# Optimization experiments

Measured on AMD Instinct MI355X. Metric: run time of the kernel, lower is better.

Reference implementation:

```python
import jax, jax.numpy as jnp
import numpy as np
import math

EPS = 1e-5

def layernorm(x, g, b):
    mu = jnp.mean(x, axis=-1, keepdims=True)
    var = jnp.var(x, axis=-1, keepdims=True)
    return (x - mu) * jax.lax.rsqrt(var + EPS) * g + b

def setup_inputs() -> dict:
    key = jax.random.key(0)
    ks = jax.random.split(key, 12)
    B, T, E, H = 4, 2048, 128, 8
    D = H * E          # 1024
    F = 4 * D          # 4096
    s = 0.02
    return {
        "X":     jax.random.normal(ks[0], (B, T, E), jnp.float32),
        "ln1_g": jnp.ones((E,), jnp.float32),
        "ln1_b": jnp.zeros((E,), jnp.float32),
        "Wq":    jax.random.normal(ks[1], (H, E, E), jnp.float32) * s,
        "bq":    jax.random.normal(ks[2], (H, E), jnp.float32) * s,
        "Wk":    jax.random.normal(ks[3], (H, E, E), jnp.float32) * s,
        "bk":    jax.random.normal(ks[4], (H, E), jnp.float32) * s,
        "Wv":    jax.random.normal(ks[5], (H, E, E), jnp.float32) * s,
        "bv":    jax.random.normal(ks[6], (H, E), jnp.float32) * s,
        "ln2_g": jnp.ones((D,), jnp.float32),
        "ln2_b": jnp.zeros((D,), jnp.float32),
        "W1":    jax.random.normal(ks[7], (D, F), jnp.float32) * s,
        "b1":    jax.random.normal(ks[8], (F,), jnp.float32) * s,
        "W2":    jax.random.normal(ks[9], (F, E), jnp.float32) * s,
        "b2":    jax.random.normal(ks[10], (E,), jnp.float32) * s,
    }

def reference(X, ln1_g, ln1_b, Wq, bq, Wk, bk, Wv, bv, ln2_g, ln2_b, W1, b1, W2, b2):
    B, T, E = X.shape
    Xn = layernorm(X, ln1_g, ln1_b)                       # [B,T,E]
    # per-head projections, vectorized over heads
    q = jnp.einsum('bte,hef->bhtf', Xn, Wq) + bq[None, :, None, :]
    k = jnp.einsum('bte,hef->bhtf', Xn, Wk) + bk[None, :, None, :]
    v = jnp.einsum('bte,hef->bhtf', Xn, Wv) + bv[None, :, None, :]
    scores = jnp.einsum('bhtf,bhsf->bhts', q, k) / math.sqrt(E)
    # causal mask: positions with s > t set to -inf (triu offset=1)
    t_idx = jnp.arange(T)
    mask = t_idx[None, :] > t_idx[:, None]                # [T,S], True above diag
    scores = jnp.where(mask[None, None], -jnp.inf, scores)
    # NOTE: original code softmaxes over dim = ndim-2, i.e. the QUERY axis
    attn = jax.nn.softmax(scores, axis=-2)
    out = jnp.einsum('bhts,bhsf->bhtf', attn, v)          # [B,H,T,E]
    # concat heads along last dim (head order preserved)
    concat = jnp.transpose(out, (0, 2, 1, 3)).reshape(B, T, -1)  # [B,T,H*E]
    h = layernorm(concat, ln2_g, ln2_b)
    mid = jax.nn.gelu(h @ W1 + b1, approximate=False)
    return mid @ W2 + b2                                   # [B,T,E]
```

## Files before the change

### kernel.cpp

```cpp
#include <hip/hip_runtime.h>
#include <hip/hip_bf16.h>
#include <math.h>

typedef __hip_bfloat16 bf16;
typedef __attribute__((ext_vector_type(8))) short short8;
typedef __attribute__((ext_vector_type(4))) float floatx4;

#define B_ 4
#define T_ 2048
#define E_ 128
#define H_ 8
#define D_ 1024
#define F_ 4096
#define M_ 8192

static __device__ __forceinline__ float b2f(bf16 v){ return __bfloat162float(v); }
static __device__ __forceinline__ bf16  f2b(float v){ return __float2bfloat16(v); }
static __device__ __forceinline__ short f2bs(float v){ bf16 h = __float2bfloat16(v); return *(short*)&h; }

static __device__ __forceinline__ void glds16(const bf16* g, void* l){
  __builtin_amdgcn_global_load_lds((const __attribute__((address_space(1))) void*)g,
                                   (__attribute__((address_space(3))) void*)l, 16, 0, 0);
}

__global__ void detect_dtype_k(const unsigned int* __restrict__ g, int* __restrict__ flag){
  if (threadIdx.x == 0) flag[0] = (g[0] == 0x3F803F80u) ? 1 : 0;
}

__global__ void convert_misc_k(const void* s0, const void* s1, const void* s2, const void* s3,
                               const void* s4, const void* s5, const void* s6, const void* s7,
                               const void* s8,
                               bf16* g1, bf16* b1, bf16* bqkv, bf16* g2, bf16* b2l,
                               bf16* bb1, bf16* bb2, const int* __restrict__ flag){
  int i = blockIdx.x * 256 + threadIdx.x;
  if (i >= 9600) return;
  int fl = flag[0];
  const void* src; bf16* dst; int off;
  if      (i <  128){ src = s0; dst = g1;          off = i;        }
  else if (i <  256){ src = s1; dst = b1;          off = i - 128;  }
  else if (i < 1280){ src = s2; dst = bqkv;        off = i - 256;  }
  else if (i < 2304){ src = s3; dst = bqkv + 1024; off = i - 1280; }
  else if (i < 3328){ src = s4; dst = bqkv + 2048; off = i - 2304; }
  else if (i < 4352){ src = s5; dst = g2;          off = i - 3328; }
  else if (i < 5376){ src = s6; dst = b2l;         off = i - 4352; }
  else if (i < 9472){ src = s7; dst = bb1;         off = i - 5376; }
  else              { src = s8; dst = bb2;         off = i - 9472; }
  dst[off] = fl ? ((const bf16*)src)[off] : f2b(((const float*)src)[off]);
}

__global__ __launch_bounds__(256) void transpose_cvt_k(const void* __restrict__ src, bf16* __restrict__ dst,
                                                       int R, int C, const int* __restrict__ flag){
  __shared__ float tile[32][33];
  int r0 = blockIdx.y * 32, c0 = blockIdx.x * 32;
  int tx = threadIdx.x & 31, ty = threadIdx.x >> 5;
  int fl = flag[0];
  #pragma unroll
  for (int i = 0; i < 32; i += 8){
    size_t idx = (size_t)(r0 + ty + i) * C + c0 + tx;
    tile[ty + i][tx] = fl ? b2f(((const bf16*)src)[idx]) : ((const float*)src)[idx];
  }
  __syncthreads();
  #pragma unroll
  for (int i = 0; i < 32; i += 8){
    dst[(size_t)(c0 + ty + i) * R + r0 + tx] = f2b(tile[tx][ty + i]);
  }
}

__global__ __launch_bounds__(256) void transpose_qkv_k(const void* __restrict__ Wq, const void* __restrict__ Wk,
                                                       const void* __restrict__ Wv, bf16* __restrict__ dst,
                                                       const int* __restrict__ flag){
  __shared__ float tile[32][33];
  int sel = blockIdx.z >> 3, h = blockIdx.z & 7;
  const void* src = (sel == 0) ? Wq : (sel == 1) ? Wk : Wv;
  size_t mo = (size_t)h * E_ * E_;
  bf16* d = dst + (size_t)sel * H_ * E_ * E_ + mo;
  int r0 = blockIdx.y * 32, c0 = blockIdx.x * 32;
  int tx = threadIdx.x & 31, ty = threadIdx.x >> 5;
  int fl = flag[0];
  #pragma unroll
  for (int i = 0; i < 32; i += 8){
    size_t idx = mo + (size_t)(r0 + ty + i) * E_ + c0 + tx;
    tile[ty + i][tx] = fl ? b2f(((const bf16*)src)[idx]) : ((const float*)src)[idx];
  }
  __syncthreads();
  #pragma unroll
  for (int i = 0; i < 32; i += 8){
    d[(size_t)(c0 + ty + i) * E_ + r0 + tx] = f2b(tile[tx][ty + i]);
  }
}

__global__ __launch_bounds__(256) void ln1_k(const void* __restrict__ X, const bf16* __restrict__ g,
                                             const bf16* __restrict__ b, bf16* __restrict__ out,
                                             const int* __restrict__ flag){
  int row = blockIdx.x * 4 + (threadIdx.x >> 6);
  int lane = threadIdx.x & 63;
  float x0, x1;
  if (flag[0]){
    const bf16* xp = (const bf16*)X + (size_t)row * E_;
    x0 = b2f(xp[lane]); x1 = b2f(xp[lane + 64]);
  } else {
    const float* xp = (const float*)X + (size_t)row * E_;
    x0 = xp[lane]; x1 = xp[lane + 64];
  }
  float s  = x0 + x1;
  float s2 = x0 * x0 + x1 * x1;
  #pragma unroll
  for (int o = 32; o > 0; o >>= 1){ s += __shfl_xor(s, o, 64); s2 += __shfl_xor(s2, o, 64); }
  float mu  = s * (1.0f / 128.0f);
  float var = s2 * (1.0f / 128.0f) - mu * mu;
  float rs  = rsqrtf(var + 1e-5f);
  out[(size_t)row * E_ + lane]      = f2b((x0 - mu) * rs * b2f(g[lane])      + b2f(b[lane]));
  out[(size_t)row * E_ + lane + 64] = f2b((x1 - mu) * rs * b2f(g[lane + 64]) + b2f(b[lane + 64]));
}

template<int EPI>
__global__ __launch_bounds__(256, 3) void gemm_mfma_k(
    const bf16* __restrict__ A, const bf16* __restrict__ Bt,
    const bf16* __restrict__ bias, void* __restrict__ out,
    int K, const int* __restrict__ flag)
{
  __shared__ __align__(16) short As[2][4][128][8];
  __shared__ __align__(16) short Bs[2][4][128][8];
  int tid = threadIdx.x;
  int lane = tid & 63, w = tid >> 6;
  int quad = lane >> 4, l16 = lane & 15;
  int wm = w & 1, wn = w >> 1;
  int m0 = blockIdx.y * 128;
  int n0, nit;
  size_t kstart;
  if (EPI == 3){ n0 = 0; int kc = K >> 3; kstart = (size_t)blockIdx.x * kc; nit = kc >> 5; }
  else         { n0 = blockIdx.x * 128; kstart = 0; nit = K >> 5; }

  int seg0 = w * 2, seg1 = w * 2 + 1;
  int kq0 = seg0 & 3, mb0 = (seg0 >> 2) * 64;
  int kq1 = seg1 & 3, mb1 = (seg1 >> 2) * 64;
  const bf16* pa0 = A  + (size_t)(m0 + mb0 + lane) * K + kstart + kq0 * 8;
  const bf16* pa1 = A  + (size_t)(m0 + mb1 + lane) * K + kstart + kq1 * 8;
  const bf16* pb0 = Bt + (size_t)(n0 + mb0 + lane) * K + kstart + kq0 * 8;
  const bf16* pb1 = Bt + (size_t)(n0 + mb1 + lane) * K + kstart + kq1 * 8;
  uint4 ra0 = *(const uint4*)pa0, ra1 = *(const uint4*)pa1;
  uint4 rb0 = *(const uint4*)pb0, rb1 = *(const uint4*)pb1;

  floatx4 acc[4][4];
  #pragma unroll
  for (int i = 0; i < 4; i++)
    #pragma unroll
    for (int j = 0; j < 4; j++) acc[i][j] = (floatx4){0.f, 0.f, 0.f, 0.f};

  for (int it = 0; it < nit; it++){
    int buf = it & 1;
    *(uint4*)&As[buf][kq0][mb0 + lane][0] = ra0;
    *(uint4*)&As[buf][kq1][mb1 + lane][0] = ra1;
    *(uint4*)&Bs[buf][kq0][mb0 + lane][0] = rb0;
    *(uint4*)&Bs[buf][kq1][mb1 + lane][0] = rb1;
    __syncthreads();
    if (it + 1 < nit){
      int ko = (it + 1) << 5;
      ra0 = *(const uint4*)(pa0 + ko); ra1 = *(const uint4*)(pa1 + ko);
      rb0 = *(const uint4*)(pb0 + ko); rb1 = *(const uint4*)(pb1 + ko);
    }
    short8 af[4], bfr[4];
    #pragma unroll
    for (int i = 0; i < 4; i++) af[i]  = *(const short8*)&As[buf][quad][wm * 64 + i * 16 + l16][0];
    #pragma unroll
    for (int j = 0; j < 4; j++) bfr[j] = *(const short8*)&Bs[buf][quad][wn * 64 + j * 16 + l16][0];
    #pragma unroll
    for (int i = 0; i < 4; i++)
      #pragma unroll
      for (int j = 0; j < 4; j++)
        acc[i][j] = __builtin_amdgcn_mfma_f32_16x16x32_bf16(af[i], bfr[j], acc[i][j], 0, 0, 0);
  }

  bf16* po = (EPI == 3) ? (bf16*)out + (size_t)blockIdx.x * M_ * E_ : nullptr;
  #pragma unroll
  for (int i = 0; i < 4; i++){
    #pragma unroll
    for (int j = 0; j < 4; j++){
      int nn = n0 + wn * 64 + j * 16 + l16;
      float bv = (EPI == 3) ? 0.0f : b2f(bias[nn]);
      if (EPI == 0){
        int sel = nn >> 10, h = (nn >> 7) & 7, f = nn & 127;
        size_t SZ = (size_t)B_ * H_ * T_ * E_;
        int mmb = m0 + wm * 64 + i * 16 + quad * 4;
        int b = mmb >> 11, t = mmb & (T_ - 1);
        if (sel < 2){
          #pragma unroll
          for (int r = 0; r < 4; r++)
            ((bf16*)out)[(size_t)sel * SZ + (((size_t)(b * H_ + h) * T_ + t + r) * E_) + f] =
              f2b(acc[i][j][r] + bv);
        } else {
          ushort4 pk;
          #pragma unroll
          for (int r = 0; r < 4; r++) ((short*)&pk)[r] = f2bs(acc[i][j][r] + bv);
          *(ushort4*)((bf16*)out + 2 * SZ + (((size_t)(b * H_ + h) * E_ + f) * T_) + t) = pk;
        }
      } else {
        #pragma unroll
        for (int r = 0; r < 4; r++){
          int mm = m0 + wm * 64 + i * 16 + quad * 4 + r;
          po[(size_t)mm * E_ + nn] = f2b(acc[i][j][r] + bv);
        }
      }
    }
  }
}

__global__ __launch_bounds__(512, 2) void mlp1_8ph_k(
    const bf16* __restrict__ A, const bf16* __restrict__ Bt,
    const bf16* __restrict__ bias, bf16* __restrict__ out)
{
  __shared__ __align__(16) short As[3][4][256][8];
  __shared__ __align__(16) short Bs[3][4][256][8];
  constexpr int K  = D_;
  constexpr int NK = K / 32;

  int tid = threadIdx.x;
  int lane = tid & 63, w = tid >> 6;
  int quad = lane >> 4, l16 = lane & 15;
  int wm = w & 1, wn = w >> 1;
  int m0 = blockIdx.y * 256, n0 = blockIdx.x * 256;

  int u0 = w * 2, u1 = u0 + 1;
  int q0 = u0 & 3, r0 = u0 >> 2;
  int q1 = u1 & 3, r1 = u1 >> 2;
  const bf16* gA0 = A  + (size_t)(m0 + r0 * 64 + lane) * K + q0 * 8;
  const bf16* gA1 = A  + (size_t)(m0 + r1 * 64 + lane) * K + q1 * 8;
  const bf16* gB0 = Bt + (size_t)(n0 + r0 * 64 + lane) * K + q0 * 8;
  const bf16* gB1 = Bt + (size_t)(n0 + r1 * 64 + lane) * K + q1 * 8;

  glds16(gA0,      &As[0][q0][r0 * 64][0]);
  glds16(gA1,      &As[0][q1][r1 * 64][0]);
  glds16(gB0,      &Bs[0][q0][r0 * 64][0]);
  glds16(gB1,      &Bs[0][q1][r1 * 64][0]);
  glds16(gA0 + 32, &As[1][q0][r0 * 64][0]);
  glds16(gA1 + 32, &As[1][q1][r1 * 64][0]);
  glds16(gB0 + 32, &Bs[1][q0][r0 * 64][0]);
  glds16(gB1 + 32, &Bs[1][q1][r1 * 64][0]);
  asm volatile("s_waitcnt vmcnt(4)" ::: "memory");
  __builtin_amdgcn_s_barrier();

  floatx4 acc[2][4][4];
  #pragma unroll
  for (int h = 0; h < 2; h++)
    #pragma unroll
    for (int i = 0; i < 4; i++)
      #pragma unroll
      for (int j = 0; j < 4; j++) acc[h][i][j] = (floatx4){0.f, 0.f, 0.f, 0.f};

  int b0 = 0;
  #pragma unroll 1
  for (int k = 0; k < NK; ++k){
    int b2 = b0 + 2; if (b2 >= 3) b2 -= 3;
    short8 af[4], bf8[4];
    #pragma unroll
    for (int i = 0; i < 4; i++) af[i]  = *(const short8*)&As[b0][quad][wm * 128 + i * 16 + l16][0];
    #pragma unroll
    for (int j = 0; j < 4; j++) bf8[j] = *(const short8*)&Bs[b0][quad][wn * 64  + j * 16 + l16][0];
    if (k + 2 < NK){
      int ko = (k + 2) * 32;
      glds16(gA0 + ko, &As[b2][q0][r0 * 64][0]);
      glds16(gA1 + ko, &As[b2][q1][r1 * 64][0]);
    }
    __builtin_amdgcn_s_barrier();
    __builtin_amdgcn_s_setprio(1);
    #pragma unroll
    for (int i = 0; i < 4; i++)
      #pragma unroll
      for (int j = 0; j < 4; j++)
        acc[0][i][j] = __builtin_amdgcn_mfma_f32_16x16x32_bf16(af[i], bf8[j], acc[0][i][j], 0, 0, 0);
    __builtin_amdgcn_s_setprio(0);
    short8 ah[4];
    #pragma unroll
    for (int i = 0; i < 4; i++) ah[i] = *(const short8*)&As[b0][quad][wm * 128 + 64 + i * 16 + l16][0];
    if (k + 2 < NK){
      int ko = (k + 2) * 32;
      glds16(gB0 + ko, &Bs[b2][q0][r0 * 64][0]);
      glds16(gB1 + ko, &Bs[b2][q1][r1 * 64][0]);
      asm volatile("s_waitcnt vmcnt(4)" ::: "memory");
    } else if (k + 1 < NK){
      asm volatile("s_waitcnt vmcnt(0)" ::: "memory");
    }
    asm volatile("s_waitcnt lgkmcnt(0)" ::: "memory");
    __builtin_amdgcn_sched_barrier(0);
    __builtin_amdgcn_s_barrier();
    __builtin_amdgcn_s_setprio(1);
    #pragma unroll
    for (int i = 0; i < 4; i++)
      #pragma unroll
      for (int j = 0; j < 4; j++)
        acc[1][i][j] = __builtin_amdgcn_mfma_f32_16x16x32_bf16(ah[i], bf8[j], acc[1][i][j], 0, 0, 0);
    __builtin_amdgcn_s_setprio(0);
    b0++; if (b0 == 3) b0 = 0;
  }

  #pragma unroll
  for (int h = 0; h < 2; h++){
    #pragma unroll
    for (int i = 0; i < 4; i++){
      #pragma unroll
      for (int j = 0; j < 4; j++){
        int nn = n0 + wn * 64 + j * 16 + l16;
        float bv = b2f(bias[nn]);
        #pragma unroll
        for (int r = 0; r < 4; r++){
          int mm = m0 + wm * 128 + h * 64 + i * 16 + quad * 4 + r;
          float v = acc[h][i][j][r] + bv;
          float e = __expf(1.5957691216057308f * v * (1.0f + 0.044715f * v * v));
          out[(size_t)mm * F_ + nn] = f2b(v - v / (1.0f + e));
        }
      }
    }
  }
}

__global__ __launch_bounds__(256) void mlp2_fin_k(const bf16* __restrict__ P, const bf16* __restrict__ bias,
                                                  void* __restrict__ out, const int* __restrict__ flag){
  int i = blockIdx.x * 256 + threadIdx.x;
  const size_t S = (size_t)M_ * E_;
  float v = b2f(bias[i & (E_ - 1)]);
  #pragma unroll
  for (int k = 0; k < 8; k++) v += b2f(P[i + k * S]);
  if (flag[0]) ((bf16*)out)[i] = f2b(v);
  else         ((float*)out)[i] = v;
}

__global__ __launch_bounds__(256, 2) void colstats_k(const bf16* __restrict__ Q, const bf16* __restrict__ K,
                                                     float* __restrict__ IL){
  __shared__ __align__(16) short Qs[2][4][4][128][8];
  __shared__ float lcol[64];
  const float scale = 0.0883883476483184f;
  int tid = threadIdx.x;
  int lane = tid & 63, w = tid >> 6;
  int quad = lane >> 4, l16 = lane & 15;
  int x = blockIdx.x;
  int c = x & 255, phase = x >> 8;
  int q = c & 7, bh = c >> 3;
  int sblk = (phase == 0) ? q : (phase == 1) ? 31 - q : (phase == 2) ? 8 + q : 23 - q;
  int s0 = sblk * 64;

  short8 bk[4][4];
  #pragma unroll
  for (int j = 0; j < 4; j++)
    #pragma unroll
    for (int kb = 0; kb < 4; kb++)
      bk[j][kb] = *(const short8*)(K + ((size_t)bh * T_ + s0 + j * 16 + l16) * E_ + kb * 32 + quad * 8);

  if (tid < 64) lcol[tid] = 0.0f;

  int t0s = (s0 / 128) * 128;
  int nit = (T_ - t0s) >> 7;

  #pragma unroll
  for (int t2 = 0; t2 < 8; t2++){
    int seg = w * 8 + t2;
    int kb = seg >> 3, kq = (seg >> 1) & 3, hf = seg & 1;
    const bf16* ga = Q + ((size_t)bh * T_ + t0s + hf * 64 + lane) * E_ + kb * 32 + kq * 8;
    __builtin_amdgcn_global_load_lds((const __attribute__((address_space(1))) void*)ga,
                                     (__attribute__((address_space(3))) void*)&Qs[0][kb][kq][hf * 64][0], 16, 0, 0);
  }
  __syncthreads();

  float part[4] = {0.f, 0.f, 0.f, 0.f};
  for (int it = 0; it < nit; it++){
    int buf = it & 1;
    if (it + 1 < nit){
      int nb = buf ^ 1;
      int t1 = t0s + ((it + 1) << 7);
      #pragma unroll
      for (int t2 = 0; t2 < 8; t2++){
        int seg = w * 8 + t2;
        int kb = seg >> 3, kq = (seg >> 1) & 3, hf = seg & 1;
        const bf16* ga = Q + ((size_t)bh * T_ + t1 + hf * 64 + lane) * E_ + kb * 32 + kq * 8;
        __builtin_amdgcn_global_load_lds((const __attribute__((address_space(1))) void*)ga,
                                         (__attribute__((address_space(3))) void*)&Qs[nb][kb][kq][hf * 64][0], 16, 0, 0);
      }
    }
    floatx4 acc[2][4];
    #pragma unroll
    for (int i = 0; i < 2; i++)
      #pragma unroll
      for (int j = 0; j < 4; j++) acc[i][j] = (floatx4){0.f, 0.f, 0.f, 0.f};
    #pragma unroll
    for (int kb = 0; kb < 4; kb++){
      short8 af[2];
      #pragma unroll
      for (int i = 0; i < 2; i++) af[i] = *(const short8*)&Qs[buf][kb][quad][w * 32 + i * 16 + l16][0];
      #pragma unroll
      for (int i = 0; i < 2; i++)
        #pragma unroll
        for (int j = 0; j < 4; j++)
          acc[i][j] = __builtin_amdgcn_mfma_f32_16x16x32_bf16(af[i], bk[j][kb], acc[i][j], 0, 0, 0);
    }
    int t0 = t0s + (it << 7);
    bool dtile = (it == 0);
    #pragma unroll
    for (int i = 0; i < 2; i++)
      #pragma unroll
      for (int j = 0; j < 4; j++)
        #pragma unroll
        for (int r = 0; r < 4; r++){
          float e = __expf(acc[i][j][r] * scale);
          if (dtile){
            int t = t0 + w * 32 + i * 16 + quad * 4 + r;
            int s = s0 + j * 16 + l16;
            if (t < s) e = 0.0f;
          }
          part[j] += e;
        }
    __syncthreads();
  }
  #pragma unroll
  for (int j = 0; j < 4; j++){
    part[j] += __shfl_xor(part[j], 16, 64);
    part[j] += __shfl_xor(part[j], 32, 64);
  }
  if (quad == 0){
    #pragma unroll
    for (int j = 0; j < 4; j++) atomicAdd(&lcol[j * 16 + l16], part[j]);
  }
  __syncthreads();
  if (tid < 64) IL[(size_t)bh * T_ + s0 + tid] = 1.0f / lcol[tid];
}

__global__ __launch_bounds__(256, 2) void attnout_k(const bf16* __restrict__ Q, const bf16* __restrict__ K,
                                                    const bf16* __restrict__ VT, const float* __restrict__ IL,
                                                    bf16* __restrict__ CC){
  __shared__ __align__(16) short Qs[128][136];
  __shared__ __align__(16) short KV[64 * 136 > 128 * 72 ? 64 * 136 : 128 * 72];
  __shared__ __align__(16) short Ps[128][72];
  const float scale = 0.0883883476483184f;
  int tid = threadIdx.x;
  int lane = tid & 63, w = tid >> 6;
  int quad = lane >> 4, l16 = lane & 15;
  int x = blockIdx.x;
  int c = x & 255, phase = x >> 8;
  int q = c & 7, bh = c >> 3;
  int tblk = phase ? (15 - q) : q;
  int t0 = tblk * 128;
  int b = bh >> 3, h = bh & 7;

  #pragma unroll
  for (int i = 0; i < 8; i++){
    int idx = tid + i * 256; int r = idx >> 4, cc = idx & 15;
    *(uint4*)&Qs[r][cc * 8] = *(const uint4*)(Q + ((size_t)bh * T_ + t0 + r) * E_ + cc * 8);
  }
  floatx4 O[2][8];
  #pragma unroll
  for (int i = 0; i < 2; i++)
    #pragma unroll
    for (int n = 0; n < 8; n++) O[i][n] = (floatx4){0.f, 0.f, 0.f, 0.f};

  for (int s0 = 0; s0 < t0 + 128; s0 += 64){
    __syncthreads();
    #pragma unroll
    for (int i = 0; i < 4; i++){
      int idx = tid + i * 256; int r = idx >> 4, cc = idx & 15;
      *(uint4*)&KV[(r) * 136 + cc * 8] = *(const uint4*)(K + ((size_t)bh * T_ + s0 + r) * E_ + cc * 8);
    }
    __syncthreads();
    floatx4 acc[2][4];
    #pragma unroll
    for (int i = 0; i < 2; i++)
      #pragma unroll
      for (int j = 0; j < 4; j++) acc[i][j] = (floatx4){0.f, 0.f, 0.f, 0.f};
    #pragma unroll
    for (int kb = 0; kb < 4; kb++){
      short8 af[2], bfr[4];
      #pragma unroll
      for (int i = 0; i < 2; i++) af[i]  = *(const short8*)&Qs[w * 32 + i * 16 + l16][kb * 32 + quad * 8];
      #pragma unroll
      for (int j = 0; j < 4; j++) bfr[j] = *(const short8*)&KV[(j * 16 + l16) * 136 + kb * 32 + quad * 8];
      #pragma unroll
      for (int i = 0; i < 2; i++)
        #pragma unroll
        for (int j = 0; j < 4; j++)
          acc[i][j] = __builtin_amdgcn_mfma_f32_16x16x32_bf16(af[i], bfr[j], acc[i][j], 0, 0, 0);
    }
    float il[4];
    #pragma unroll
    for (int j = 0; j < 4; j++) il[j] = IL[(size_t)bh * T_ + s0 + j * 16 + l16];
    bool dtile = (s0 + 63 > t0);
    #pragma unroll
    for (int i = 0; i < 2; i++)
      #pragma unroll
      for (int j = 0; j < 4; j++)
        #pragma unroll
        for (int r = 0; r < 4; r++){
          float p = __expf(acc[i][j][r] * scale) * il[j];
          int trow = w * 32 + i * 16 + quad * 4 + r;
          if (dtile){
            int t = t0 + trow, s = s0 + j * 16 + l16;
            if (t < s) p = 0.0f;
          }
          Ps[trow][j * 16 + l16] = f2bs(p);
        }
    __syncthreads();
    #pragma unroll
    for (int i = 0; i < 4; i++){
      int idx = tid + i * 256; int e = idx >> 3, cc = idx & 7;
      *(uint4*)&KV[e * 72 + cc * 8] = *(const uint4*)(VT + ((size_t)bh * E_ + e) * T_ + s0 + cc * 8);
    }
    __syncthreads();
    #pragma unroll
    for (int kb2 = 0; kb2 < 2; kb2++){
      short8 pa[2], vb[8];
      #pragma unroll
      for (int i = 0; i < 2; i++) pa[i] = *(const short8*)&Ps[w * 32 + i * 16 + l16][kb2 * 32 + quad * 8];
      #pragma unroll
      for (int n = 0; n < 8; n++) vb[n] = *(const short8*)&KV[(n * 16 + l16) * 72 + kb2 * 32 + quad * 8];
      #pragma unroll
      for (int i = 0; i < 2; i++)
        #pragma unroll
        for (int n = 0; n < 8; n++)
          O[i][n] = __builtin_amdgcn_mfma_f32_16x16x32_bf16(pa[i], vb[n], O[i][n], 0, 0, 0);
    }
  }
  #pragma unroll
  for (int i = 0; i < 2; i++)
    #pragma unroll
    for (int n = 0; n < 8; n++)
      #pragma unroll
      for (int r = 0; r < 4; r++){
        int t = t0 + w * 32 + i * 16 + quad * 4 + r;
        int e = n * 16 + l16;
        CC[((size_t)(b * T_ + t)) * D_ + h * E_ + e] = f2b(O[i][n][r]);
      }
}

__global__ __launch_bounds__(256) void ln2_k(const bf16* __restrict__ in, const bf16* __restrict__ g,
                                             const bf16* __restrict__ bta, bf16* __restrict__ out){
  __shared__ float wsum[4], wsum2[4];
  int row = blockIdx.x, tid = threadIdx.x;
  const bf16* xp = in + (size_t)row * D_;
  float x[4]; float s = 0.0f, s2 = 0.0f;
  #pragma unroll
  for (int i = 0; i < 4; i++){ x[i] = b2f(xp[tid + i * 256]); s += x[i]; s2 += x[i] * x[i]; }
  #pragma unroll
  for (int o = 32; o > 0; o >>= 1){ s += __shfl_xor(s, o, 64); s2 += __shfl_xor(s2, o, 64); }
  int wid = tid >> 6;
  if ((tid & 63) == 0){ wsum[wid] = s; wsum2[wid] = s2; }
  __syncthreads();
  s  = wsum[0] + wsum[1] + wsum[2] + wsum[3];
  s2 = wsum2[0] + wsum2[1] + wsum2[2] + wsum2[3];
  float mu  = s * (1.0f / 1024.0f);
  float var = s2 * (1.0f / 1024.0f) - mu * mu;
  float rs  = rsqrtf(var + 1e-5f);
  #pragma unroll
  for (int i = 0; i < 4; i++){
    int c = tid + i * 256;
    out[(size_t)row * D_ + c] = f2b((x[i] - mu) * rs * b2f(g[c]) + b2f(bta[c]));
  }
}

static constexpr size_t A256(size_t x){ return (x + 255) & ~(size_t)255; }

extern "C" void kernel_launch(void* const* d_in, const int* in_sizes, int n_in,
                              void* d_out, int out_size, void* d_ws, size_t ws_size,
                              hipStream_t stream){
  (void)in_sizes; (void)n_in; (void)out_size; (void)ws_size;
  char* ws = (char*)d_ws;

  constexpr size_t o_flag  = 0;
  constexpr size_t o_g1    = 256;
  constexpr size_t o_b1    = A256(o_g1    + (size_t)E_ * 2);
  constexpr size_t o_WqkvT = A256(o_b1    + (size_t)E_ * 2);
  constexpr size_t o_bqkv  = A256(o_WqkvT + (size_t)3 * H_ * E_ * E_ * 2);
  constexpr size_t o_g2    = A256(o_bqkv  + (size_t)3 * H_ * E_ * 2);
  constexpr size_t o_b2l   = A256(o_g2    + (size_t)D_ * 2);
  constexpr size_t o_W1T   = A256(o_b2l   + (size_t)D_ * 2);
  constexpr size_t o_bb1   = A256(o_W1T   + (size_t)D_ * F_ * 2);
  constexpr size_t o_W2T   = A256(o_bb1   + (size_t)F_ * 2);
  constexpr size_t o_bb2   = A256(o_W2T   + (size_t)F_ * E_ * 2);
  constexpr size_t o_xn    = A256(o_bb2   + (size_t)E_ * 2);
  constexpr size_t o_q     = A256(o_xn    + (size_t)M_ * E_ * 2);
  constexpr size_t o_k     = o_q + (size_t)B_ * H_ * T_ * E_ * 2;
  constexpr size_t o_vt    = o_k + (size_t)B_ * H_ * T_ * E_ * 2;
  constexpr size_t o_il    = A256(o_vt + (size_t)B_ * H_ * T_ * E_ * 2);
  constexpr size_t o_cc    = A256(o_il + (size_t)B_ * H_ * T_ * 4);
  constexpr size_t o_h2    = A256(o_cc + (size_t)M_ * D_ * 2);
  constexpr size_t o_mid   = o_q;
  constexpr size_t o_part  = o_h2;
  static_assert(o_mid + (size_t)M_ * F_ * 2 <= o_h2, "mid overlaps live h2 buffer");
  static_assert((size_t)8 * M_ * E_ * 2 <= (size_t)M_ * D_ * 2, "partials exceed h2 region");

  int*  flag  = (int*)(ws + o_flag);
  bf16* g1    = (bf16*)(ws + o_g1);
  bf16* b1p   = (bf16*)(ws + o_b1);
  bf16* WqkvT = (bf16*)(ws + o_WqkvT);
  bf16* bqkv  = (bf16*)(ws + o_bqkv);
  bf16* g2    = (bf16*)(ws + o_g2);
  bf16* b2l   = (bf16*)(ws + o_b2l);
  bf16* W1T   = (bf16*)(ws + o_W1T);
  bf16* bb1   = (bf16*)(ws + o_bb1);
  bf16* W2T   = (bf16*)(ws + o_W2T);
  bf16* bb2   = (bf16*)(ws + o_bb2);
  bf16* xn    = (bf16*)(ws + o_xn);
  bf16* Qb    = (bf16*)(ws + o_q);
  bf16* Kb    = (bf16*)(ws + o_k);
  bf16* VTb   = (bf16*)(ws + o_vt);
  float* ILp  = (float*)(ws + o_il);
  bf16* ccp   = (bf16*)(ws + o_cc);
  bf16* h2p   = (bf16*)(ws + o_h2);
  bf16* midp  = (bf16*)(ws + o_mid);
  bf16* part  = (bf16*)(ws + o_part);

  detect_dtype_k<<<1, 64, 0, stream>>>((const unsigned int*)d_in[1], flag);

  convert_misc_k<<<38, 256, 0, stream>>>(d_in[1], d_in[2], d_in[4], d_in[6], d_in[8],
                                         d_in[9], d_in[10], d_in[12], d_in[14],
                                         g1, b1p, bqkv, g2, b2l, bb1, bb2, flag);

  transpose_qkv_k<<<dim3(4, 4, 24), 256, 0, stream>>>(d_in[3], d_in[5], d_in[7], WqkvT, flag);
  transpose_cvt_k<<<dim3(F_ / 32, D_ / 32), 256, 0, stream>>>(d_in[11], W1T, D_, F_, flag);
  transpose_cvt_k<<<dim3(E_ / 32, F_ / 32), 256, 0, stream>>>(d_in[13], W2T, F_, E_, flag);

  ln1_k<<<M_ / 4, 256, 0, stream>>>(d_in[0], g1, b1p, xn, flag);

  gemm_mfma_k<0><<<dim3(3 * D_ / 128, M_ / 128), 256, 0, stream>>>(xn, WqkvT, bqkv, Qb, E_, flag);

  colstats_k<<<1024, 256, 0, stream>>>(Qb, Kb, ILp);
  attnout_k<<<512, 256, 0, stream>>>(Qb, Kb, VTb, ILp, ccp);

  ln2_k<<<M_, 256, 0, stream>>>(ccp, g2, b2l, h2p);

  mlp1_8ph_k<<<dim3(F_ / 256, M_ / 256), 512, 0, stream>>>(h2p, W1T, bb1, midp);
  gemm_mfma_k<3><<<dim3(8, M_ / 128), 256, 0, stream>>>(midp, W2T, bb2, part, F_, flag);
  mlp2_fin_k<<<M_ * E_ / 256, 256, 0, stream>>>(part, bb2, d_out, flag);
}
```

Before: 419.1 us.

## Restructure MLP1 GEMM into a single-phase, four-stage LDS pipeline

```diff
diff --git a/kernel.cpp b/kernel.cpp
--- a/kernel.cpp
+++ b/kernel.cpp
@@ -205,12 +205,12 @@
   }
 }
 
-__global__ __launch_bounds__(512, 2) void mlp1_8ph_k(
+__global__ __launch_bounds__(512, 2) void mlp1_1ph_k(
     const bf16* __restrict__ A, const bf16* __restrict__ Bt,
     const bf16* __restrict__ bias, bf16* __restrict__ out)
 {
-  __shared__ __align__(16) short As[3][4][256][8];
-  __shared__ __align__(16) short Bs[3][4][256][8];
+  __shared__ __align__(16) short As[4][4][256][8];
+  __shared__ __align__(16) short Bs[4][4][256][8];
   constexpr int K  = D_;
   constexpr int NK = K / 32;
 
@@ -228,15 +228,15 @@
   const bf16* gB0 = Bt + (size_t)(n0 + r0 * 64 + lane) * K + q0 * 8;
   const bf16* gB1 = Bt + (size_t)(n0 + r1 * 64 + lane) * K + q1 * 8;
 
-  glds16(gA0,      &As[0][q0][r0 * 64][0]);
-  glds16(gA1,      &As[0][q1][r1 * 64][0]);
-  glds16(gB0,      &Bs[0][q0][r0 * 64][0]);
-  glds16(gB1,      &Bs[0][q1][r1 * 64][0]);
-  glds16(gA0 + 32, &As[1][q0][r0 * 64][0]);
-  glds16(gA1 + 32, &As[1][q1][r1 * 64][0]);
-  glds16(gB0 + 32, &Bs[1][q0][r0 * 64][0]);
-  glds16(gB1 + 32, &Bs[1][q1][r1 * 64][0]);
-  asm volatile("s_waitcnt vmcnt(4)" ::: "memory");
+  #pragma unroll
+  for (int t = 0; t < 3; t++){
+    int ko = t * 32;
+    glds16(gA0 + ko, &As[t][q0][r0 * 64][0]);
+    glds16(gA1 + ko, &As[t][q1][r1 * 64][0]);
+    glds16(gB0 + ko, &Bs[t][q0][r0 * 64][0]);
+    glds16(gB1 + ko, &Bs[t][q1][r1 * 64][0]);
+  }
+  asm volatile("s_waitcnt vmcnt(8)" ::: "memory");
   __builtin_amdgcn_s_barrier();
 
   floatx4 acc[2][4][4];
@@ -247,50 +247,38 @@
       #pragma unroll
       for (int j = 0; j < 4; j++) acc[h][i][j] = (floatx4){0.f, 0.f, 0.f, 0.f};
 
-  int b0 = 0;
   #pragma unroll 1
   for (int k = 0; k < NK; ++k){
-    int b2 = b0 + 2; if (b2 >= 3) b2 -= 3;
-    short8 af[4], bf8[4];
-    #pragma unroll
-    for (int i = 0; i < 4; i++) af[i]  = *(const short8*)&As[b0][quad][wm * 128 + i * 16 + l16][0];
-    #pragma unroll
-    for (int j = 0; j < 4; j++) bf8[j] = *(const short8*)&Bs[b0][quad][wn * 64  + j * 16 + l16][0];
-    if (k + 2 < NK){
-      int ko = (k + 2) * 32;
-      glds16(gA0 + ko, &As[b2][q0][r0 * 64][0]);
-      glds16(gA1 + ko, &As[b2][q1][r1 * 64][0]);
-    }
-    __builtin_amdgcn_s_barrier();
+    int bk = k & 3, b3 = (k + 3) & 3;
+    short8 bf8[4], a2[2][4];
+    #pragma unroll
+    for (int j = 0; j < 4; j++) bf8[j]   = *(const short8*)&Bs[bk][quad][wn * 64  + j * 16 + l16][0];
+    #pragma unroll
+    for (int i = 0; i < 4; i++) a2[0][i] = *(const short8*)&As[bk][quad][wm * 128 + i * 16 + l16][0];
+    #pragma unroll
+    for (int i = 0; i < 4; i++) a2[1][i] = *(const short8*)&As[bk][quad][wm * 128 + 64 + i * 16 + l16][0];
+    if (k + 3 < NK){
+      int ko = (k + 3) * 32;
+      glds16(gA0 + ko, &As[b3][q0][r0 * 64][0]);
+      glds16(gA1 + ko, &As[b3][q1][r1 * 64][0]);
+      glds16(gB0 + ko, &Bs[b3][q0][r0 * 64][0]);
+      glds16(gB1 + ko, &Bs[b3][q1][r1 * 64][0]);
+    }
     __builtin_amdgcn_s_setprio(1);
     #pragma unroll
-    for (int i = 0; i < 4; i++)
-      #pragma unroll
-      for (int j = 0; j < 4; j++)
-        acc[0][i][j] = __builtin_amdgcn_mfma_f32_16x16x32_bf16(af[i], bf8[j], acc[0][i][j], 0, 0, 0);
+    for (int h = 0; h < 2; h++)
+      #pragma unroll
+      for (int i = 0; i < 4; i++)
+        #pragma unroll
+        for (int j = 0; j < 4; j++)
+          acc[h][i][j] = __builtin_amdgcn_mfma_f32_16x16x32_bf16(a2[h][i], bf8[j], acc[h][i][j], 0, 0, 0);
     __builtin_amdgcn_s_setprio(0);
-    short8 ah[4];
-    #pragma unroll
-    for (int i = 0; i < 4; i++) ah[i] = *(const short8*)&As[b0][quad][wm * 128 + 64 + i * 16 + l16][0];
-    if (k + 2 < NK){
-      int ko = (k + 2) * 32;
-      glds16(gB0 + ko, &Bs[b2][q0][r0 * 64][0]);
-      glds16(gB1 + ko, &Bs[b2][q1][r1 * 64][0]);
-      asm volatile("s_waitcnt vmcnt(4)" ::: "memory");
-    } else if (k + 1 < NK){
-      asm volatile("s_waitcnt vmcnt(0)" ::: "memory");
-    }
+    if (k < NK - 3)       { asm volatile("s_waitcnt vmcnt(8)" ::: "memory"); }
+    else if (k == NK - 3) { asm volatile("s_waitcnt vmcnt(4)" ::: "memory"); }
+    else if (k == NK - 2) { asm volatile("s_waitcnt vmcnt(0)" ::: "memory"); }
     asm volatile("s_waitcnt lgkmcnt(0)" ::: "memory");
     __builtin_amdgcn_sched_barrier(0);
     __builtin_amdgcn_s_barrier();
-    __builtin_amdgcn_s_setprio(1);
-    #pragma unroll
-    for (int i = 0; i < 4; i++)
-      #pragma unroll
-      for (int j = 0; j < 4; j++)
-        acc[1][i][j] = __builtin_amdgcn_mfma_f32_16x16x32_bf16(ah[i], bf8[j], acc[1][i][j], 0, 0, 0);
-    __builtin_amdgcn_s_setprio(0);
-    b0++; if (b0 == 3) b0 = 0;
   }
 
   #pragma unroll
@@ -623,7 +611,7 @@
 
   ln2_k<<<M_, 256, 0, stream>>>(ccp, g2, b2l, h2p);
 
-  mlp1_8ph_k<<<dim3(F_ / 256, M_ / 256), 512, 0, stream>>>(h2p, W1T, bb1, midp);
+  mlp1_1ph_k<<<dim3(F_ / 256, M_ / 256), 512, 0, stream>>>(h2p, W1T, bb1, midp);
   gemm_mfma_k<3><<<dim3(8, M_ / 128), 256, 0, stream>>>(midp, W2T, bb2, part, F_, flag);
   mlp2_fin_k<<<M_ * E_ / 256, 256, 0, stream>>>(part, bb2, d_out, flag);
 }
```

Result: no change. 420.2 us (+0.3%).
